# Optimization experiments

Measured on AMD Instinct MI355X. Metric: run time of the kernel, lower is better.

The kernel has to match this reference:

```python
import jax, jax.numpy as jnp
from jax import lax
import numpy as np

THRESH = 0.5
R = 4  # suppression radius -> (2R+1)^3 max-pool window


def setup_inputs() -> dict:
    key = jax.random.key(0)
    pred_vol = jax.random.uniform(key, (1, 1, 64, 512, 512), dtype=jnp.float32)
    return {"pred_vol": pred_vol}


def reference(pred_vol):
    # Threshold: keep values above thresh, zero otherwise
    pred_thresh = jnp.where(pred_vol > THRESH, pred_vol, jnp.float32(0.0))
    # 3D max-pool, kernel 2R+1, stride 1, padding R (pad with -inf so padding
    k = 2 * R + 1
    conf = lax.reduce_window(
        pred_thresh,
        -jnp.inf,
        lax.max,
        window_dimensions=(1, 1, k, k, k),
        window_strides=(1, 1, 1, 1, 1),
        padding=[(0, 0), (0, 0), (R, R), (R, R), (R, R)],
    )
    # Keep only strict local maxima of the thresholded volume
    conf = jnp.where((conf > 0.0) & (conf == pred_thresh), conf, jnp.float32(0.0))
    return jnp.squeeze(conf)  # [D, H, W]
```

## Files before the change

### kernel.cpp

```cpp
#include <hip/hip_runtime.h>

static constexpr int Dd = 64;
static constexpr int Hh = 512;
static constexpr int Ww = 512;
static constexpr int RAD = 4;
static constexpr float THRESH_V = 0.5f;
static constexpr int W4 = Ww / 4;
static constexpr int PLANE4 = Hh * W4;

static constexpr int TH = 4;
static constexpr int DC = 16;
static constexpr int ROWS = TH + 2 * RAD;
static constexpr int STEPS = DC + 2 * RAD;
static constexpr int NBLK = (Hh / TH) * (Dd / DC);

typedef float nf4 __attribute__((ext_vector_type(4)));

__device__ __forceinline__ float4 f4max(float4 a, float4 b) {
    return make_float4(fmaxf(a.x, b.x), fmaxf(a.y, b.y), fmaxf(a.z, b.z), fmaxf(a.w, b.w));
}
__device__ __forceinline__ int iclamp(int v, int lo, int hi) {
    return v < lo ? lo : (v > hi ? hi : v);
}

#define BAR_VM(N) asm volatile("s_waitcnt vmcnt(" #N ") lgkmcnt(0)\n\ts_barrier" ::: "memory")
#define BAR_LDS() asm volatile("s_waitcnt lgkmcnt(0)\n\ts_barrier" ::: "memory")

__device__ __forceinline__ void load_lds16(const float4* g, float4* l) {
    __builtin_amdgcn_global_load_lds(
        (const __attribute__((address_space(1))) void*)g,
        (__attribute__((address_space(3))) void*)l, 16, 0, 0);
}

__global__ __launch_bounds__(512, 2)
void fused_nms_k(const float4* __restrict__ x4, float4* __restrict__ o4) {
    __shared__ float4 braw[2][ROWS * W4];
    __shared__ float4 bcol[TH * W4];

    const int tid  = threadIdx.x;
    const int w4   = tid & (W4 - 1);
    const int hr   = tid >> 7;
    const int wid  = tid >> 6;
    const int lane = tid & 63;

    const int b    = blockIdx.x;
    const int band = b & 7;
    const int rest = b >> 3;
    const int ht   = band * 16 + (rest & 15);
    const int dc   = rest >> 4;
    const int h0   = ht * TH;
    const int d0   = dc * DC;

    const int colm = w4 ? w4 - 1 : 0;
    const int colp = (w4 < W4 - 1) ? w4 + 1 : W4 - 1;
    const int outrow = (h0 + hr) * W4 + w4;

    int goff[3], loff[3];
#pragma unroll
    for (int k = 0; k < 3; ++k) {
        const int s    = wid + 8 * k;
        const int row  = s >> 1;
        const int half = s & 1;
        const int gh   = iclamp(h0 - RAD + row, 0, Hh - 1);
        goff[k] = gh * W4 + half * 64 + lane;
        loff[k] = row * W4 + half * 64;
    }

    auto stage = [&](int t, int par) {
        const int gd = iclamp(d0 - RAD + t, 0, Dd - 1);
        const float4* pl = x4 + (size_t)gd * PLANE4;
#pragma unroll
        for (int k = 0; k < 3; ++k)
            load_lds16(pl + goff[k], &braw[par][loff[k]]);
    };

    float4 R[8];

    auto body = [&](int t, int slot, int par, bool emit, bool emitPrev) {
        if (emitPrev) BAR_VM(1); else BAR_VM(0);

        float4 cen;
        if (emit) {
            cen = x4[(size_t)(d0 + t - 2 * RAD) * PLANE4 + outrow];
            __builtin_amdgcn_sched_barrier(0);
        }
        if (t + 1 < STEPS) stage(t + 1, par ^ 1);

        const float4* Bc = &braw[par][hr * W4 + w4];
        float4 m = f4max(Bc[0 * W4], Bc[1 * W4]);
        m = f4max(m, f4max(Bc[2 * W4], Bc[3 * W4]));
        m = f4max(m, f4max(Bc[4 * W4], Bc[5 * W4]));
        m = f4max(m, f4max(Bc[6 * W4], Bc[7 * W4]));
        m = f4max(m, Bc[8 * W4]);
        bcol[hr * W4 + w4] = m;
        BAR_LDS();

        const float4 lmv = bcol[hr * W4 + colm];
        const float4 rmv = bcol[hr * W4 + colp];
        const float l3 = lmv.w, l2 = fmaxf(lmv.z, l3), l1 = fmaxf(lmv.y, l2), l0 = fmaxf(lmv.x, l1);
        const float core = fmaxf(fmaxf(m.x, m.y), fmaxf(m.z, m.w));
        const float r0 = rmv.x, r1 = fmaxf(r0, rmv.y), r2 = fmaxf(r1, rmv.z), r3 = fmaxf(r2, rmv.w);
        float4 pm;
        pm.x = fmaxf(l0, fmaxf(core, r0));
        pm.y = fmaxf(l1, fmaxf(core, r1));
        pm.z = fmaxf(l2, fmaxf(core, r2));
        pm.w = fmaxf(l3, fmaxf(core, r3));

        if (emit) {
            float4 mm = pm;
#pragma unroll
            for (int i = 0; i < 8; ++i) mm = f4max(mm, R[i]);
            nf4 q;
            q.x = (cen.x > THRESH_V && cen.x == mm.x) ? cen.x : 0.0f;
            q.y = (cen.y > THRESH_V && cen.y == mm.y) ? cen.y : 0.0f;
            q.z = (cen.z > THRESH_V && cen.z == mm.z) ? cen.z : 0.0f;
            q.w = (cen.w > THRESH_V && cen.w == mm.w) ? cen.w : 0.0f;
            __builtin_nontemporal_store(
                q, (nf4*)&o4[(size_t)(d0 + t - 2 * RAD) * PLANE4 + outrow]);
        }
        R[slot] = pm;
    };

    stage(0, 0);
#pragma unroll
    for (int t = 0; t < 8; ++t) body(t, t, t & 1, false, false);
    body(8, 0, 0, true, false);
#pragma unroll
    for (int j = 1; j < 8; ++j) body(8 + j, j, j & 1, true, true);
#pragma unroll
    for (int j = 0; j < 8; ++j) body(16 + j, j, j & 1, true, true);
}

extern "C" void kernel_launch(void* const* d_in, const int* in_sizes, int n_in,
                              void* d_out, int out_size, void* d_ws, size_t ws_size,
                              hipStream_t stream) {
    const float4* x4 = (const float4*)d_in[0];
    float4* out4 = (float4*)d_out;
    (void)d_ws; (void)ws_size; (void)in_sizes; (void)n_in; (void)out_size;
    fused_nms_k<<<dim3(NBLK), dim3(512), 0, stream>>>(x4, out4);
}
```

Baseline: 123.8 us.

## Software-pipeline vertical and horizontal max stages with one wave computing vertical pooling

Restructures the per-plane loop so the vertical (H) max over the 12 staged rows is computed once per plane by 128 threads, which share the 6-row core across the 4 output rows. The results go into a double-buffered column buffer, and the horizontal pass consumes the previous plane's result. This removes one barrier per step and redundant vertical reads, letting vertical, horizontal and DMA stages overlap across iterations. In exchange, only a quarter of the threads do the vertical work, so that part may serialize. A leftover unused kernel and an undefined entry declaration remain.

After: 125.1 us. No clear change (+1.0%).

```diff
diff --git a/kernel.cpp b/kernel.cpp
--- a/kernel.cpp
+++ b/kernel.cpp
@@ -11,7 +11,7 @@
 static constexpr int TH = 4;
 static constexpr int DC = 16;
 static constexpr int ROWS = TH + 2 * RAD;
-static constexpr int STEPS = DC + 2 * RAD;
+static constexpr int NPL = DC + 2 * RAD;
 static constexpr int NBLK = (Hh / TH) * (Dd / DC);
 
 typedef float nf4 __attribute__((ext_vector_type(4)));
@@ -35,7 +35,7 @@
 __global__ __launch_bounds__(512, 2)
 void fused_nms_k(const float4* __restrict__ x4, float4* __restrict__ o4) {
     __shared__ float4 braw[2][ROWS * W4];
-    __shared__ float4 bcol[TH * W4];
+    __shared__ float4 bcol[2][TH * W4];
 
     const int tid  = threadIdx.x;
     const int w4   = tid & (W4 - 1);
@@ -66,69 +66,209 @@
         loff[k] = row * W4 + half * 64;
     }
 
-    auto stage = [&](int t, int par) {
-        const int gd = iclamp(d0 - RAD + t, 0, Dd - 1);
+    auto stage = [&](int p) {
+        const int gd = iclamp(d0 - RAD + p, 0, Dd - 1);
         const float4* pl = x4 + (size_t)gd * PLANE4;
 #pragma unroll
         for (int k = 0; k < 3; ++k)
-            load_lds16(pl + goff[k], &braw[par][loff[k]]);
+            load_lds16(pl + goff[k], &braw[p & 1][loff[k]]);
+    };
+
+    auto vert = [&](int p) {
+        if (tid < W4) {
+            const float4* B = &braw[p & 1][tid];
+            float4 core = f4max(f4max(f4max(B[3 * W4], B[4 * W4]),
+                                      f4max(B[5 * W4], B[6 * W4])),
+                                f4max(B[7 * W4], B[8 * W4]));
+            float4 q0 = B[0], q1 = B[1 * W4], q2 = B[2 * W4];
+            float4 q9 = B[9 * W4], q10 = B[10 * W4], q11 = B[11 * W4];
+            float4 b12 = f4max(q1, q2), c910 = f4max(q9, q10);
+            float4* O = &bcol[p & 1][tid];
+            O[0 * W4] = f4max(core, f4max(q0, b12));
+            O[1 * W4] = f4max(core, f4max(b12, q9));
+            O[2 * W4] = f4max(core, f4max(q2, c910));
+            O[3 * W4] = f4max(core, f4max(c910, q11));
+        }
     };
 
     float4 R[8];
 
-    auto body = [&](int t, int slot, int par, bool emit, bool emitPrev) {
-        if (emitPrev) BAR_VM(1); else BAR_VM(0);
+#pragma unroll
+    for (int t = 0; t <= NPL; ++t) {
+        const bool doH   = (t >= 1);
+        const bool doE   = (t >= 9);
+        const bool doV   = (t <= NPL - 1);
+        const bool doDMA = (t <= NPL - 2);
 
         float4 cen;
-        if (emit) {
-            cen = x4[(size_t)(d0 + t - 2 * RAD) * PLANE4 + outrow];
+        if (doE) {
+            cen = x4[(size_t)(d0 + t - 9) * PLANE4 + outrow];
             __builtin_amdgcn_sched_barrier(0);
         }
-        if (t + 1 < STEPS) stage(t + 1, par ^ 1);
-
-        const float4* Bc = &braw[par][hr * W4 + w4];
-        float4 m = f4max(Bc[0 * W4], Bc[1 * W4]);
-        m = f4max(m, f4max(Bc[2 * W4], Bc[3 * W4]));
-        m = f4max(m, f4max(Bc[4 * W4], Bc[5 * W4]));
-        m = f4max(m, f4max(Bc[6 * W4], Bc[7 * W4]));
-        m = f4max(m, Bc[8 * W4]);
-        bcol[hr * W4 + w4] = m;
-        BAR_LDS();
-
-        const float4 lmv = bcol[hr * W4 + colm];
-        const float4 rmv = bcol[hr * W4 + colp];
-        const float l3 = lmv.w, l2 = fmaxf(lmv.z, l3), l1 = fmaxf(lmv.y, l2), l0 = fmaxf(lmv.x, l1);
-        const float core = fmaxf(fmaxf(m.x, m.y), fmaxf(m.z, m.w));
-        const float r0 = rmv.x, r1 = fmaxf(r0, rmv.y), r2 = fmaxf(r1, rmv.z), r3 = fmaxf(r2, rmv.w);
-        float4 pm;
-        pm.x = fmaxf(l0, fmaxf(core, r0));
-        pm.y = fmaxf(l1, fmaxf(core, r1));
-        pm.z = fmaxf(l2, fmaxf(core, r2));
-        pm.w = fmaxf(l3, fmaxf(core, r3));
-
-        if (emit) {
-            float4 mm = pm;
-#pragma unroll
-            for (int i = 0; i < 8; ++i) mm = f4max(mm, R[i]);
-            nf4 q;
-            q.x = (cen.x > THRESH_V && cen.x == mm.x) ? cen.x : 0.0f;
-            q.y = (cen.y > THRESH_V && cen.y == mm.y) ? cen.y : 0.0f;
-            q.z = (cen.z > THRESH_V && cen.z == mm.z) ? cen.z : 0.0f;
-            q.w = (cen.w > THRESH_V && cen.w == mm.w) ? cen.w : 0.0f;
-            __builtin_nontemporal_store(
-                q, (nf4*)&o4[(size_t)(d0 + t - 2 * RAD) * PLANE4 + outrow]);
-        }
-        R[slot] = pm;
-    };
-
-    stage(0, 0);
-#pragma unroll
-    for (int t = 0; t < 8; ++t) body(t, t, t & 1, false, false);
-    body(8, 0, 0, true, false);
-#pragma unroll
-    for (int j = 1; j < 8; ++j) body(8 + j, j, j & 1, true, true);
-#pragma unroll
-    for (int j = 0; j < 8; ++j) body(16 + j, j, j & 1, true, true);
+        if (doDMA) stage(t + 1);
+
+        if (doV) vert(t);
+
+        if (doH) {
+            const float4* Bc = &bcol[(t - 1) & 1][hr * W4];
+            const float4 lm = Bc[colm], cm = Bc[w4], rm = Bc[colp];
+            const float l3 = lm.w, l2 = fmaxf(lm.z, l3), l1 = fmaxf(lm.y, l2), l0 = fmaxf(lm.x, l1);
+            const float core = fmaxf(fmaxf(cm.x, cm.y), fmaxf(cm.z, cm.w));
+            const float r0 = rm.x, r1 = fmaxf(r0, rm.y), r2 = fmaxf(r1, rm.z), r3 = fmaxf(r2, rm.w);
+            float4 pm;
+            pm.x = fmaxf(l0, fmaxf(core, r0));
+            pm.y = fmaxf(l1, fmaxf(core, r1));
+            pm.z = fmaxf(l2, fmaxf(core, r2));
+            pm.w = fmaxf(l3, fmaxf(core, r3));
+
+            if (doE) {
+                float4 mm = pm;
+#pragma unroll
+                for (int i = 0; i < 8; ++i) mm = f4max(mm, R[i]);
+                nf4 q;
+                q.x = (cen.x > THRESH_V && cen.x == mm.x) ? cen.x : 0.0f;
+                q.y = (cen.y > THRESH_V && cen.y == mm.y) ? cen.y : 0.0f;
+                q.z = (cen.z > THRESH_V && cen.z == mm.z) ? cen.z : 0.0f;
+                q.w = (cen.w > THRESH_V && cen.w == mm.w) ? cen.w : 0.0f;
+                __builtin_nontemporal_store(
+                    q, (nf4*)&o4[(size_t)(d0 + t - 9) * PLANE4 + outrow]);
+            }
+            R[(t - 1) & 7] = pm;
+        }
+
+        if (t == 0) {
+            BAR_VM(0);
+        } else if (t <= 8) {
+            BAR_VM(0);
+        } else if (doDMA) {
+            BAR_VM(1);
+        } else if (t == NPL - 1) {
+            BAR_LDS();
+        }
+    }
+}
+
+__global__ __launch_bounds__(512, 2)
+void fused_nms_entry(const float4* __restrict__ x4, float4* __restrict__ o4);
+
+extern "C" void kernel_launch(void* const* d_in, const int* in_sizes, int n_in,
+                              void* d_out, int out_size, void* d_ws, size_t ws_size,
+                              hipStream_t stream);
+
+__global__ __launch_bounds__(512, 2)
+void fused_nms_k2(const float4* __restrict__ x4, float4* __restrict__ o4) {
+    __shared__ float4 braw[2][ROWS * W4];
+    __shared__ float4 bcol[2][TH * W4];
+
+    const int tid  = threadIdx.x;
+    const int w4   = tid & (W4 - 1);
+    const int hr   = tid >> 7;
+    const int wid  = tid >> 6;
+    const int lane = tid & 63;
+
+    const int b    = blockIdx.x;
+    const int band = b & 7;
+    const int rest = b >> 3;
+    const int ht   = band * 16 + (rest & 15);
+    const int dc   = rest >> 4;
+    const int h0   = ht * TH;
+    const int d0   = dc * DC;
+
+    const int colm = w4 ? w4 - 1 : 0;
+    const int colp = (w4 < W4 - 1) ? w4 + 1 : W4 - 1;
+    const int outrow = (h0 + hr) * W4 + w4;
+
+    int goff[3], loff[3];
+#pragma unroll
+    for (int k = 0; k < 3; ++k) {
+        const int s    = wid + 8 * k;
+        const int row  = s >> 1;
+        const int half = s & 1;
+        const int gh   = iclamp(h0 - RAD + row, 0, Hh - 1);
+        goff[k] = gh * W4 + half * 64 + lane;
+        loff[k] = row * W4 + half * 64;
+    }
+
+    auto stage = [&](int p) {
+        const int gd = iclamp(d0 - RAD + p, 0, Dd - 1);
+        const float4* pl = x4 + (size_t)gd * PLANE4;
+#pragma unroll
+        for (int k = 0; k < 3; ++k)
+            load_lds16(pl + goff[k], &braw[p & 1][loff[k]]);
+    };
+
+    auto vert = [&](int p) {
+        if (tid < W4) {
+            const float4* B = &braw[p & 1][tid];
+            float4 core = f4max(f4max(f4max(B[3 * W4], B[4 * W4]),
+                                      f4max(B[5 * W4], B[6 * W4])),
+                                f4max(B[7 * W4], B[8 * W4]));
+            float4 q0 = B[0], q1 = B[1 * W4], q2 = B[2 * W4];
+            float4 q9 = B[9 * W4], q10 = B[10 * W4], q11 = B[11 * W4];
+            float4 b12 = f4max(q1, q2), c910 = f4max(q9, q10);
+            float4* O = &bcol[p & 1][tid];
+            O[0 * W4] = f4max(core, f4max(q0, b12));
+            O[1 * W4] = f4max(core, f4max(b12, q9));
+            O[2 * W4] = f4max(core, f4max(q2, c910));
+            O[3 * W4] = f4max(core, f4max(c910, q11));
+        }
+    };
+
+    float4 R[8];
+
+    stage(0);
+    BAR_VM(0);
+
+#pragma unroll
+    for (int t = 0; t <= NPL; ++t) {
+        const bool doH   = (t >= 1);
+        const bool doE   = (t >= 9);
+        const bool doV   = (t <= NPL - 1);
+        const bool doDMA = (t <= NPL - 2);
+
+        float4 cen;
+        if (doE) {
+            cen = x4[(size_t)(d0 + t - 9) * PLANE4 + outrow];
+            __builtin_amdgcn_sched_barrier(0);
+        }
+        if (doDMA) stage(t + 1);
+        if (doV) vert(t);
+
+        if (doH) {
+            const float4* Bc = &bcol[(t - 1) & 1][hr * W4];
+            const float4 lm = Bc[colm], cm = Bc[w4], rm = Bc[colp];
+            const float l3 = lm.w, l2 = fmaxf(lm.z, l3), l1 = fmaxf(lm.y, l2), l0 = fmaxf(lm.x, l1);
+            const float core = fmaxf(fmaxf(cm.x, cm.y), fmaxf(cm.z, cm.w));
+            const float r0 = rm.x, r1 = fmaxf(r0, rm.y), r2 = fmaxf(r1, rm.z), r3 = fmaxf(r2, rm.w);
+            float4 pm;
+            pm.x = fmaxf(l0, fmaxf(core, r0));
+            pm.y = fmaxf(l1, fmaxf(core, r1));
+            pm.z = fmaxf(l2, fmaxf(core, r2));
+            pm.w = fmaxf(l3, fmaxf(core, r3));
+
+            if (doE) {
+                float4 mm = pm;
+#pragma unroll
+                for (int i = 0; i < 8; ++i) mm = f4max(mm, R[i]);
+                nf4 q;
+                q.x = (cen.x > THRESH_V && cen.x == mm.x) ? cen.x : 0.0f;
+                q.y = (cen.y > THRESH_V && cen.y == mm.y) ? cen.y : 0.0f;
+                q.z = (cen.z > THRESH_V && cen.z == mm.z) ? cen.z : 0.0f;
+                q.w = (cen.w > THRESH_V && cen.w == mm.w) ? cen.w : 0.0f;
+                __builtin_nontemporal_store(
+                    q, (nf4*)&o4[(size_t)(d0 + t - 9) * PLANE4 + outrow]);
+            }
+            R[(t - 1) & 7] = pm;
+        }
+
+        if (t <= 8) {
+            BAR_VM(0);
+        } else if (doDMA) {
+            BAR_VM(1);
+        } else if (t == NPL - 1) {
+            BAR_LDS();
+        }
+    }
 }
 
 extern "C" void kernel_launch(void* const* d_in, const int* in_sizes, int n_in,
@@ -137,5 +277,5 @@
     const float4* x4 = (const float4*)d_in[0];
     float4* out4 = (float4*)d_out;
     (void)d_ws; (void)ws_size; (void)in_sizes; (void)n_in; (void)out_size;
-    fused_nms_k<<<dim3(NBLK), dim3(512), 0, stream>>>(x4, out4);
-}
+    fused_nms_k2<<<dim3(NBLK), dim3(512), 0, stream>>>(x4, out4);
+}
```

## Skew vertical and horizontal max stages with triple-buffered LDS and direct row loads

Applied to the files above, without the earlier changes.

Only the first 9 of the 12 halo rows are staged through LDS via async global-to-LDS copies. Each thread loads its last 3 vertical rows straight from global into registers. LDS staging becomes a triple buffer with two planes of prefetch, and the column buffer is double-buffered. The horizontal pass for plane t-1 now runs in the same step as the vertical pass for plane t, which removes the second barrier per plane. This cuts LDS traffic and barrier stalls, at the cost of extra direct global loads, more LDS space and more complex vmcnt accounting.

Result: slower. 131.0 us (+5.9%).

```diff
diff --git a/kernel.cpp b/kernel.cpp
--- a/kernel.cpp
+++ b/kernel.cpp
@@ -10,8 +10,8 @@
 
 static constexpr int TH = 4;
 static constexpr int DC = 16;
-static constexpr int ROWS = TH + 2 * RAD;
-static constexpr int STEPS = DC + 2 * RAD;
+static constexpr int SROWS = 9;
+static constexpr int NPL = DC + 2 * RAD;
 static constexpr int NBLK = (Hh / TH) * (Dd / DC);
 
 typedef float nf4 __attribute__((ext_vector_type(4)));
@@ -24,7 +24,6 @@
 }
 
 #define BAR_VM(N) asm volatile("s_waitcnt vmcnt(" #N ") lgkmcnt(0)\n\ts_barrier" ::: "memory")
-#define BAR_LDS() asm volatile("s_waitcnt lgkmcnt(0)\n\ts_barrier" ::: "memory")
 
 __device__ __forceinline__ void load_lds16(const float4* g, float4* l) {
     __builtin_amdgcn_global_load_lds(
@@ -33,9 +32,9 @@
 }
 
 __global__ __launch_bounds__(512, 2)
-void fused_nms_k(const float4* __restrict__ x4, float4* __restrict__ o4) {
-    __shared__ float4 braw[2][ROWS * W4];
-    __shared__ float4 bcol[TH * W4];
+void fused_nms_k4(const float4* __restrict__ x4, float4* __restrict__ o4) {
+    __shared__ float4 braw[3][SROWS * W4];
+    __shared__ float4 bcol[2][TH * W4];
 
     const int tid  = threadIdx.x;
     const int w4   = tid & (W4 - 1);
@@ -58,7 +57,7 @@
     int goff[3], loff[3];
 #pragma unroll
     for (int k = 0; k < 3; ++k) {
-        const int s    = wid + 8 * k;
+        const int s    = (k < 2) ? (wid + 8 * k) : (16 + wid);
         const int row  = s >> 1;
         const int half = s & 1;
         const int gh   = iclamp(h0 - RAD + row, 0, Hh - 1);
@@ -66,69 +65,96 @@
         loff[k] = row * W4 + half * 64;
     }
 
-    auto stage = [&](int t, int par) {
-        const int gd = iclamp(d0 - RAD + t, 0, Dd - 1);
+    int ghoff[3];
+#pragma unroll
+    for (int i = 0; i < 3; ++i) {
+        const int gh = iclamp(h0 - RAD + hr + 6 + i, 0, Hh - 1);
+        ghoff[i] = gh * W4 + w4;
+    }
+
+    auto stage = [&](int p) {
+        const int gd = iclamp(d0 - RAD + p, 0, Dd - 1);
         const float4* pl = x4 + (size_t)gd * PLANE4;
-#pragma unroll
-        for (int k = 0; k < 3; ++k)
-            load_lds16(pl + goff[k], &braw[par][loff[k]]);
+        float4* dst = braw[p % 3];
+        load_lds16(pl + goff[0], dst + loff[0]);
+        load_lds16(pl + goff[1], dst + loff[1]);
+        if (wid < 2) load_lds16(pl + goff[2], dst + loff[2]);
     };
 
     float4 R[8];
+    float4 vprev;
 
-    auto body = [&](int t, int slot, int par, bool emit, bool emitPrev) {
-        if (emitPrev) BAR_VM(1); else BAR_VM(0);
+    stage(0);
+    stage(1);
 
+#pragma unroll
+    for (int t = 0; t <= NPL; ++t) {
+        const bool doV   = (t <= NPL - 1);
+        const bool doDMA = (t <= NPL - 3);
+        const bool doH   = (t >= 1);
+        const bool doE   = (t >= 9);
+
+        if (t <= 9)       { BAR_VM(2); }
+        else if (t <= 22) { BAR_VM(3); }
+        else              { BAR_VM(1); }
+
+        float4 g0, g1, g2;
+        if (doV) {
+            const int gd = iclamp(d0 - RAD + t, 0, Dd - 1);
+            const float4* pl = x4 + (size_t)gd * PLANE4;
+            g0 = pl[ghoff[0]];
+            g1 = pl[ghoff[1]];
+            g2 = pl[ghoff[2]];
+        }
+        __builtin_amdgcn_sched_barrier(0);
         float4 cen;
-        if (emit) {
-            cen = x4[(size_t)(d0 + t - 2 * RAD) * PLANE4 + outrow];
-            __builtin_amdgcn_sched_barrier(0);
+        if (doE) cen = x4[(size_t)(d0 + t - 9) * PLANE4 + outrow];
+        __builtin_amdgcn_sched_barrier(0);
+        if (doDMA) stage(t + 2);
+        __builtin_amdgcn_sched_barrier(0);
+
+        float4 vown;
+        if (doV) {
+            const float4* Bc = &braw[t % 3][hr * W4 + w4];
+            float4 m01 = f4max(Bc[0 * W4], Bc[1 * W4]);
+            float4 m23 = f4max(Bc[2 * W4], Bc[3 * W4]);
+            float4 m45 = f4max(Bc[4 * W4], Bc[5 * W4]);
+            float4 mg  = f4max(f4max(g0, g1), g2);
+            vown = f4max(f4max(m01, m23), f4max(m45, mg));
+            bcol[t & 1][hr * W4 + w4] = vown;
         }
-        if (t + 1 < STEPS) stage(t + 1, par ^ 1);
 
-        const float4* Bc = &braw[par][hr * W4 + w4];
-        float4 m = f4max(Bc[0 * W4], Bc[1 * W4]);
-        m = f4max(m, f4max(Bc[2 * W4], Bc[3 * W4]));
-        m = f4max(m, f4max(Bc[4 * W4], Bc[5 * W4]));
-        m = f4max(m, f4max(Bc[6 * W4], Bc[7 * W4]));
-        m = f4max(m, Bc[8 * W4]);
-        bcol[hr * W4 + w4] = m;
-        BAR_LDS();
+        if (doH) {
+            const float4* Bp = &bcol[(t - 1) & 1][hr * W4];
+            const float4 lm = Bp[colm];
+            const float4 rm = Bp[colp];
+            const float4 cm = vprev;
+            const float l3 = lm.w, l2 = fmaxf(lm.z, l3), l1 = fmaxf(lm.y, l2), l0 = fmaxf(lm.x, l1);
+            const float core = fmaxf(fmaxf(cm.x, cm.y), fmaxf(cm.z, cm.w));
+            const float r0 = rm.x, r1 = fmaxf(r0, rm.y), r2 = fmaxf(r1, rm.z), r3 = fmaxf(r2, rm.w);
+            float4 pm;
+            pm.x = fmaxf(l0, fmaxf(core, r0));
+            pm.y = fmaxf(l1, fmaxf(core, r1));
+            pm.z = fmaxf(l2, fmaxf(core, r2));
+            pm.w = fmaxf(l3, fmaxf(core, r3));
 
-        const float4 lmv = bcol[hr * W4 + colm];
-        const float4 rmv = bcol[hr * W4 + colp];
-        const float l3 = lmv.w, l2 = fmaxf(lmv.z, l3), l1 = fmaxf(lmv.y, l2), l0 = fmaxf(lmv.x, l1);
-        const float core = fmaxf(fmaxf(m.x, m.y), fmaxf(m.z, m.w));
-        const float r0 = rmv.x, r1 = fmaxf(r0, rmv.y), r2 = fmaxf(r1, rmv.z), r3 = fmaxf(r2, rmv.w);
-        float4 pm;
-        pm.x = fmaxf(l0, fmaxf(core, r0));
-        pm.y = fmaxf(l1, fmaxf(core, r1));
-        pm.z = fmaxf(l2, fmaxf(core, r2));
-        pm.w = fmaxf(l3, fmaxf(core, r3));
+            if (doE) {
+                float4 mm = pm;
+#pragma unroll
+                for (int i = 0; i < 8; ++i) mm = f4max(mm, R[i]);
+                nf4 q;
+                q.x = (cen.x > THRESH_V && cen.x == mm.x) ? cen.x : 0.0f;
+                q.y = (cen.y > THRESH_V && cen.y == mm.y) ? cen.y : 0.0f;
+                q.z = (cen.z > THRESH_V && cen.z == mm.z) ? cen.z : 0.0f;
+                q.w = (cen.w > THRESH_V && cen.w == mm.w) ? cen.w : 0.0f;
+                __builtin_nontemporal_store(
+                    q, (nf4*)&o4[(size_t)(d0 + t - 9) * PLANE4 + outrow]);
+            }
+            R[(t - 1) & 7] = pm;
+        }
 
-        if (emit) {
-            float4 mm = pm;
-#pragma unroll
-            for (int i = 0; i < 8; ++i) mm = f4max(mm, R[i]);
-            nf4 q;
-            q.x = (cen.x > THRESH_V && cen.x == mm.x) ? cen.x : 0.0f;
-            q.y = (cen.y > THRESH_V && cen.y == mm.y) ? cen.y : 0.0f;
-            q.z = (cen.z > THRESH_V && cen.z == mm.z) ? cen.z : 0.0f;
-            q.w = (cen.w > THRESH_V && cen.w == mm.w) ? cen.w : 0.0f;
-            __builtin_nontemporal_store(
-                q, (nf4*)&o4[(size_t)(d0 + t - 2 * RAD) * PLANE4 + outrow]);
-        }
-        R[slot] = pm;
-    };
-
-    stage(0, 0);
-#pragma unroll
-    for (int t = 0; t < 8; ++t) body(t, t, t & 1, false, false);
-    body(8, 0, 0, true, false);
-#pragma unroll
-    for (int j = 1; j < 8; ++j) body(8 + j, j, j & 1, true, true);
-#pragma unroll
-    for (int j = 0; j < 8; ++j) body(16 + j, j, j & 1, true, true);
+        if (doV) vprev = vown;
+    }
 }
 
 extern "C" void kernel_launch(void* const* d_in, const int* in_sizes, int n_in,
@@ -137,5 +163,5 @@
     const float4* x4 = (const float4*)d_in[0];
     float4* out4 = (float4*)d_out;
     (void)d_ws; (void)ws_size; (void)in_sizes; (void)n_in; (void)out_size;
-    fused_nms_k<<<dim3(NBLK), dim3(512), 0, stream>>>(x4, out4);
+    fused_nms_k4<<<dim3(NBLK), dim3(512), 0, stream>>>(x4, out4);
 }
```

## Triple-buffer LDS plane staging and reuse staged center values

Applied to the files above, without the earlier changes.

Raw-plane staging into LDS goes from a double buffer to a three-slot ring, so each plane is prefetched two steps ahead. The waitcnt thresholds are retuned so the in-flight loads and stores are counted correctly. The center value for the local-max comparison now comes from the staged LDS row, held in a four-entry register ring, instead of a second global load per output. The extra LDS buffer brings per-block LDS to about 82 KB, so two blocks of 512 threads may no longer fit on one CU, which could cut occupancy.

Result: faster. 114.9 us (-7.2%).

```diff
diff --git a/kernel.cpp b/kernel.cpp
--- a/kernel.cpp
+++ b/kernel.cpp
@@ -11,7 +11,7 @@
 static constexpr int TH = 4;
 static constexpr int DC = 16;
 static constexpr int ROWS = TH + 2 * RAD;
-static constexpr int STEPS = DC + 2 * RAD;
+static constexpr int NPL = DC + 2 * RAD;
 static constexpr int NBLK = (Hh / TH) * (Dd / DC);
 
 typedef float nf4 __attribute__((ext_vector_type(4)));
@@ -33,8 +33,8 @@
 }
 
 __global__ __launch_bounds__(512, 2)
-void fused_nms_k(const float4* __restrict__ x4, float4* __restrict__ o4) {
-    __shared__ float4 braw[2][ROWS * W4];
+void fused_nms_k5(const float4* __restrict__ x4, float4* __restrict__ o4) {
+    __shared__ float4 braw[3][ROWS * W4];
     __shared__ float4 bcol[TH * W4];
 
     const int tid  = threadIdx.x;
@@ -66,47 +66,55 @@
         loff[k] = row * W4 + half * 64;
     }
 
-    auto stage = [&](int t, int par) {
-        const int gd = iclamp(d0 - RAD + t, 0, Dd - 1);
+    auto stage = [&](int p) {
+        const int gd = iclamp(d0 - RAD + p, 0, Dd - 1);
         const float4* pl = x4 + (size_t)gd * PLANE4;
+        float4* dst = braw[p % 3];
 #pragma unroll
         for (int k = 0; k < 3; ++k)
-            load_lds16(pl + goff[k], &braw[par][loff[k]]);
+            load_lds16(pl + goff[k], dst + loff[k]);
     };
 
     float4 R[8];
+    float4 C[4];
 
-    auto body = [&](int t, int slot, int par, bool emit, bool emitPrev) {
-        if (emitPrev) BAR_VM(1); else BAR_VM(0);
+    stage(0);
+    stage(1);
 
-        float4 cen;
-        if (emit) {
-            cen = x4[(size_t)(d0 + t - 2 * RAD) * PLANE4 + outrow];
-            __builtin_amdgcn_sched_barrier(0);
-        }
-        if (t + 1 < STEPS) stage(t + 1, par ^ 1);
+#pragma unroll
+    for (int t = 0; t < NPL; ++t) {
+        const bool doE = (t >= 8);
 
-        const float4* Bc = &braw[par][hr * W4 + w4];
-        float4 m = f4max(Bc[0 * W4], Bc[1 * W4]);
-        m = f4max(m, f4max(Bc[2 * W4], Bc[3 * W4]));
-        m = f4max(m, f4max(Bc[4 * W4], Bc[5 * W4]));
-        m = f4max(m, f4max(Bc[6 * W4], Bc[7 * W4]));
-        m = f4max(m, Bc[8 * W4]);
+        if (t <= 8)       { BAR_VM(3); }
+        else if (t == 9)  { BAR_VM(4); }
+        else if (t <= 22) { BAR_VM(5); }
+        else              { BAR_VM(2); }
+
+        if (t + 2 < NPL) stage(t + 2);
+        __builtin_amdgcn_sched_barrier(0);
+
+        const float4* Bc = &braw[t % 3][hr * W4 + w4];
+        float4 q0 = Bc[0 * W4], q1 = Bc[1 * W4], q2 = Bc[2 * W4], q3 = Bc[3 * W4];
+        float4 c4 = Bc[4 * W4];
+        float4 q5 = Bc[5 * W4], q6 = Bc[6 * W4], q7 = Bc[7 * W4], q8 = Bc[8 * W4];
+        float4 m = f4max(f4max(f4max(q0, q1), f4max(q2, q3)),
+                         f4max(f4max(c4, q5), f4max(f4max(q6, q7), q8)));
         bcol[hr * W4 + w4] = m;
         BAR_LDS();
 
-        const float4 lmv = bcol[hr * W4 + colm];
-        const float4 rmv = bcol[hr * W4 + colp];
-        const float l3 = lmv.w, l2 = fmaxf(lmv.z, l3), l1 = fmaxf(lmv.y, l2), l0 = fmaxf(lmv.x, l1);
+        const float4 lm = bcol[hr * W4 + colm];
+        const float4 rm = bcol[hr * W4 + colp];
+        const float l3 = lm.w, l2 = fmaxf(lm.z, l3), l1 = fmaxf(lm.y, l2), l0 = fmaxf(lm.x, l1);
         const float core = fmaxf(fmaxf(m.x, m.y), fmaxf(m.z, m.w));
-        const float r0 = rmv.x, r1 = fmaxf(r0, rmv.y), r2 = fmaxf(r1, rmv.z), r3 = fmaxf(r2, rmv.w);
+        const float r0 = rm.x, r1 = fmaxf(r0, rm.y), r2 = fmaxf(r1, rm.z), r3 = fmaxf(r2, rm.w);
         float4 pm;
         pm.x = fmaxf(l0, fmaxf(core, r0));
         pm.y = fmaxf(l1, fmaxf(core, r1));
         pm.z = fmaxf(l2, fmaxf(core, r2));
         pm.w = fmaxf(l3, fmaxf(core, r3));
 
-        if (emit) {
+        if (doE) {
+            const float4 cen = C[t & 3];
             float4 mm = pm;
 #pragma unroll
             for (int i = 0; i < 8; ++i) mm = f4max(mm, R[i]);
@@ -116,19 +124,11 @@
             q.z = (cen.z > THRESH_V && cen.z == mm.z) ? cen.z : 0.0f;
             q.w = (cen.w > THRESH_V && cen.w == mm.w) ? cen.w : 0.0f;
             __builtin_nontemporal_store(
-                q, (nf4*)&o4[(size_t)(d0 + t - 2 * RAD) * PLANE4 + outrow]);
+                q, (nf4*)&o4[(size_t)(d0 + t - 8) * PLANE4 + outrow]);
         }
-        R[slot] = pm;
-    };
-
-    stage(0, 0);
-#pragma unroll
-    for (int t = 0; t < 8; ++t) body(t, t, t & 1, false, false);
-    body(8, 0, 0, true, false);
-#pragma unroll
-    for (int j = 1; j < 8; ++j) body(8 + j, j, j & 1, true, true);
-#pragma unroll
-    for (int j = 0; j < 8; ++j) body(16 + j, j, j & 1, true, true);
+        R[t & 7] = pm;
+        C[t & 3] = c4;
+    }
 }
 
 extern "C" void kernel_launch(void* const* d_in, const int* in_sizes, int n_in,
@@ -137,5 +137,5 @@
     const float4* x4 = (const float4*)d_in[0];
     float4* out4 = (float4*)d_out;
     (void)d_ws; (void)ws_size; (void)in_sizes; (void)n_in; (void)out_size;
-    fused_nms_k<<<dim3(NBLK), dim3(512), 0, stream>>>(x4, out4);
+    fused_nms_k5<<<dim3(NBLK), dim3(512), 0, stream>>>(x4, out4);
 }
```
